# Optimization experiments

Measured on AMD Instinct MI355X. Metric: run time of the kernel, lower is better.

Reference implementation:

```python
import jax, jax.numpy as jnp
import numpy as np

E = 256; D = 512; A = 5; NS = 2048; NQ = 8192; NWAY = 5
_OTHERS = np.array([[j for j in range(A) if j != i] for i in range(A)])  # [A, A-1] indices of other agents
_ROWS = np.arange(A)[:, None]


def _ln(x, g, b, eps=1e-5):
    m = x.mean(-1, keepdims=True)
    v = ((x - m) ** 2).mean(-1, keepdims=True)
    return (x - m) * jax.lax.rsqrt(v + eps) * g + b


def _mha(x, in_w, in_b, out_w, out_b, h, mask=None):
    # torch nn.MultiheadAttention (batch_first) self-attention. in_w: [3E,E], out_w: [E,E]
    B, S, Em = x.shape
    hd = Em // h
    qkv = x @ in_w.T + in_b
    q, k, v = jnp.split(qkv, 3, axis=-1)
    q = q.reshape(B, S, h, hd).transpose(0, 2, 1, 3) * (1.0 / np.sqrt(hd))
    k = k.reshape(B, S, h, hd).transpose(0, 2, 1, 3)
    v = v.reshape(B, S, h, hd).transpose(0, 2, 1, 3)
    s = jnp.einsum('bhqd,bhkd->bhqk', q, k)
    if mask is not None:
        s = jnp.where(mask, s, jnp.asarray(-1e9, s.dtype))
    a = jax.nn.softmax(s, axis=-1)
    o = jnp.einsum('bhqk,bhkd->bhqd', a, v).transpose(0, 2, 1, 3).reshape(B, S, Em)
    return o @ out_w.T + out_b


def _forward(support_x, support_y, query_x, n_way, fe0_w1, fe0_b1, fe0_g1, fe0_be1, fe0_w2, fe0_b2, fe0_g2, fe0_be2, fe1_w1, fe1_b1, fe1_g, fe1_be, fe1_w2, fe1_b2, fe2_w1, fe2_b1, fe2_w2, fe2_b2, fe2_g, fe2_be, fe3_w1, fe3_b1, fe3_w2, fe3_b2, fe3_g, fe3_be, fe4_w1, fe4_b1, fe4_w2, fe4_b2, fe4_w3, fe4_b3, msg_enc_w, msg_enc_b, agg_in_w, agg_in_b, agg_out_w, agg_out_b, proc_w1, proc_b1, proc_w2, proc_b2, internal_state, proto_in_w, proto_in_b, proto_out_w, proto_out_b, cls_w1, cls_b1, cls_w2, cls_b2, cls_w3, cls_b3, comm_w, f_w1, f_b1, f_w2, f_b2, f_w3, f_b3):
    # --- per-agent-type feature extractors (eval mode: dropout off) ---
    def fe0(x):
        h = jax.nn.relu(_ln(x @ fe0_w1 + fe0_b1, fe0_g1, fe0_be1))
        return jax.nn.relu(_ln(h @ fe0_w2 + fe0_b2, fe0_g2, fe0_be2))
    def fe1(x):
        h = jax.nn.relu(_ln(x @ fe1_w1 + fe1_b1, fe1_g, fe1_be))
        return jnp.tanh(h @ fe1_w2 + fe1_b2)
    def fe2(x):
        h = jax.nn.relu(x @ fe2_w1 + fe2_b1)
        return jax.nn.relu(_ln(h @ fe2_w2 + fe2_b2, fe2_g, fe2_be))
    def fe3(x):
        h = jax.nn.relu(x @ fe3_w1 + fe3_b1)
        return jax.nn.sigmoid(_ln(h @ fe3_w2 + fe3_b2, fe3_g, fe3_be))
    def fe4(x):
        h = jax.nn.relu(x @ fe4_w1 + fe4_b1)
        h = jax.nn.relu(h @ fe4_w2 + fe4_b2)
        return h @ fe4_w3 + fe4_b3
    feats_s = jnp.stack([fe0(support_x), fe1(support_x), fe2(support_x), fe3(support_x), fe4(support_x)])  # [A,NS,E]
    feats_q = jnp.stack([fe0(query_x), fe1(query_x), fe2(query_x), fe3(query_x), fe4(query_x)])            # [A,NQ,E]

    # --- one communication round: generate -> weight -> MHA-aggregate -> MLP-process ---
    agent_state = feats_s.mean(1) + internal_state                                         # [A,E]
    messages = jnp.tanh(jnp.einsum('ae,aef->af', agent_state, msg_enc_w) + msg_enc_b)      # [A,E]
    wgt = jax.nn.softmax(comm_w, axis=-1)                                                  # [A,A]
    msgs = messages[_OTHERS] * wgt[_ROWS, _OTHERS][..., None]                              # [A,A-1,E]
    def agg_one(m, iw, ib, ow, ob):
        return _mha(m[None], iw, ib, ow, ob, 4)[0].mean(0)
    agg = jax.vmap(agg_one)(msgs, agg_in_w, agg_in_b, agg_out_w, agg_out_b)                # [A,E]
    comb = internal_state + agg
    hh = jax.nn.relu(jnp.einsum('ae,aef->af', comb, proc_w1) + proc_b1)
    ck = jnp.einsum('ae,aef->af', hh, proc_w2) + proc_b2                                   # [A,E] communicated knowledge

    # --- class-masked prototype attention (equivalent to per-class MHA) + logits ---
    mask = support_y[:, None] == support_y[None, :]                                        # [NS,NS]
    counts = jax.ops.segment_sum(jnp.ones(support_y.shape, jnp.float32), support_y, num_segments=n_way)
    def head(fs, fq, cki, piw, pib, pw, pb, c1, c1b, c2, c2b, c3, c3b):
        att = _mha((fs + cki[None])[None], piw, pib, pw, pb, 2, mask[None, None])[0]       # [NS,E]
        psum = jax.ops.segment_sum(att, support_y, num_segments=n_way)
        protos = jnp.where(counts[:, None] > 0, psum / jnp.maximum(counts, 1.0)[:, None], 0.0)  # [n_way,E]
        eq = jnp.concatenate([fq, jnp.broadcast_to(cki, fq.shape)], axis=-1)               # [NQ,2E]
        d2 = (fq * fq).sum(-1, keepdims=True) + (protos * protos).sum(-1)[None, :] - 2.0 * (fq @ protos.T)
        dist = jnp.sqrt(jnp.maximum(d2, 1e-12))                                            # cdist
        c = jax.nn.relu(eq @ c1 + c1b)
        c = jax.nn.relu(c @ c2 + c2b)
        conf = c @ c3 + c3b                                                                # [NQ,1]
        return -dist + conf * 0.1
    logits = jax.vmap(head)(feats_s, feats_q, ck, proto_in_w, proto_in_b, proto_out_w, proto_out_b, cls_w1, cls_b1, cls_w2, cls_b2, cls_w3, cls_b3)  # [A,NQ,n_way]

    # --- decision fusion over concatenated per-agent query features ---
    qcat = feats_q.transpose(1, 0, 2).reshape(NQ, A * E)
    fh = jax.nn.relu(qcat @ f_w1 + f_b1)
    fh = jax.nn.relu(fh @ f_w2 + f_b2)
    fused = fh @ f_w3 + f_b3                                                               # [NQ,1]
    return logits, fused


def setup_inputs() -> dict:
    key = jax.random.key(0)
    ks = iter(jax.random.split(key, 80))
    def rn(shape, scale=1.0):
        return (jax.random.normal(next(ks), shape) * scale).astype(jnp.float32)
    def lin(shape, fan):
        return rn(shape, 1.0 / np.sqrt(fan))
    z = lambda s: jnp.zeros(s, jnp.float32)
    o = lambda s: jnp.ones(s, jnp.float32)
    inp = {}
    inp['support_x'] = rn((NS, D))
    inp['support_y'] = jax.random.randint(next(ks), (NS,), 0, NWAY, dtype=jnp.int32)
    inp['query_x'] = rn((NQ, D))
    inp['n_way'] = NWAY
    inp['fe0_w1'] = lin((D, 2 * E), D); inp['fe0_b1'] = z((2 * E,)); inp['fe0_g1'] = o((2 * E,)); inp['fe0_be1'] = z((2 * E,))
    inp['fe0_w2'] = lin((2 * E, E), 2 * E); inp['fe0_b2'] = z((E,)); inp['fe0_g2'] = o((E,)); inp['fe0_be2'] = z((E,))
    inp['fe1_w1'] = lin((D, E), D); inp['fe1_b1'] = z((E,)); inp['fe1_g'] = o((E,)); inp['fe1_be'] = z((E,))
    inp['fe1_w2'] = lin((E, E), E); inp['fe1_b2'] = z((E,))
    inp['fe2_w1'] = lin((D, 3 * E), D); inp['fe2_b1'] = z((3 * E,))
    inp['fe2_w2'] = lin((3 * E, E), 3 * E); inp['fe2_b2'] = z((E,)); inp['fe2_g'] = o((E,)); inp['fe2_be'] = z((E,))
    inp['fe3_w1'] = lin((D, E), D); inp['fe3_b1'] = z((E,))
    inp['fe3_w2'] = lin((E, E), E); inp['fe3_b2'] = z((E,)); inp['fe3_g'] = o((E,)); inp['fe3_be'] = z((E,))
    inp['fe4_w1'] = lin((D, 2 * E), D); inp['fe4_b1'] = z((2 * E,))
    inp['fe4_w2'] = lin((2 * E, E), 2 * E); inp['fe4_b2'] = z((E,))
    inp['fe4_w3'] = lin((E, E), E); inp['fe4_b3'] = z((E,))
    inp['msg_enc_w'] = lin((A, E, E), E); inp['msg_enc_b'] = z((A, E))
    inp['agg_in_w'] = lin((A, 3 * E, E), E); inp['agg_in_b'] = z((A, 3 * E))
    inp['agg_out_w'] = lin((A, E, E), E); inp['agg_out_b'] = z((A, E))
    inp['proc_w1'] = lin((A, E, E), E); inp['proc_b1'] = z((A, E))
    inp['proc_w2'] = lin((A, E, E), E); inp['proc_b2'] = z((A, E))
    inp['internal_state'] = rn((A, E), 0.01)
    inp['proto_in_w'] = lin((A, 3 * E, E), E); inp['proto_in_b'] = z((A, 3 * E))
    inp['proto_out_w'] = lin((A, E, E), E); inp['proto_out_b'] = z((A, E))
    inp['cls_w1'] = lin((A, 2 * E, E), 2 * E); inp['cls_b1'] = z((A, E))
    inp['cls_w2'] = lin((A, E, E // 2), E); inp['cls_b2'] = z((A, E // 2))
    inp['cls_w3'] = lin((A, E // 2, 1), E // 2); inp['cls_b3'] = z((A, 1))
    inp['comm_w'] = (jnp.eye(A) * 0.5 + 0.1).astype(jnp.float32)
    inp['f_w1'] = lin((A * E, E), A * E); inp['f_b1'] = z((E,))
    inp['f_w2'] = lin((E, E // 2), E); inp['f_b2'] = z((E // 2,))
    inp['f_w3'] = lin((E // 2, 1), E // 2); inp['f_b3'] = z((1,))
    return inp


def reference(support_x, support_y, query_x, n_way, fe0_w1, fe0_b1, fe0_g1, fe0_be1, fe0_w2, fe0_b2, fe0_g2, fe0_be2, fe1_w1, fe1_b1, fe1_g, fe1_be, fe1_w2, fe1_b2, fe2_w1, fe2_b1, fe2_w2, fe2_b2, fe2_g, fe2_be, fe3_w1, fe3_b1, fe3_w2, fe3_b2, fe3_g, fe3_be, fe4_w1, fe4_b1, fe4_w2, fe4_b2, fe4_w3, fe4_b3, msg_enc_w, msg_enc_b, agg_in_w, agg_in_b, agg_out_w, agg_out_b, proc_w1, proc_b1, proc_w2, proc_b2, internal_state, proto_in_w, proto_in_b, proto_out_w, proto_out_b, cls_w1, cls_b1, cls_w2, cls_b2, cls_w3, cls_b3, comm_w, f_w1, f_b1, f_w2, f_b2, f_w3, f_b3):
    return _forward(support_x, support_y, query_x, n_way, fe0_w1, fe0_b1, fe0_g1, fe0_be1, fe0_w2, fe0_b2, fe0_g2, fe0_be2, fe1_w1, fe1_b1, fe1_g, fe1_be, fe1_w2, fe1_b2, fe2_w1, fe2_b1, fe2_w2, fe2_b2, fe2_g, fe2_be, fe3_w1, fe3_b1, fe3_w2, fe3_b2, fe3_g, fe3_be, fe4_w1, fe4_b1, fe4_w2, fe4_b2, fe4_w3, fe4_b3, msg_enc_w, msg_enc_b, agg_in_w, agg_in_b, agg_out_w, agg_out_b, proc_w1, proc_b1, proc_w2, proc_b2, internal_state, proto_in_w, proto_in_b, proto_out_w, proto_out_b, cls_w1, cls_b1, cls_w2, cls_b2, cls_w3, cls_b3, comm_w, f_w1, f_b1, f_w2, f_b2, f_w3, f_b3)
```

## Files before the change

### kernel.cpp

```cpp
#include <hip/hip_runtime.h>
#include <hip/hip_bf16.h>

typedef __hip_bfloat16 bf16;
typedef short s8v __attribute__((ext_vector_type(8)));
typedef short s4v __attribute__((ext_vector_type(4)));
typedef float f4v __attribute__((ext_vector_type(4)));

#define A_  5
#define D_  512
#define E_  256
#define NS_ 2048
#define NQ_ 8192
#define NM_ 10240
#define NWAY_ 5
#define QSCALE 0.088388347648318447f
#define FSTR ((size_t)NM_ * E_)

__device__ inline float ldw(const void* p, size_t i, int f32) {
  return f32 ? ((const float*)p)[i] : __bfloat162float(((const bf16*)p)[i]);
}
template<bool DYN>
__device__ inline float ldT(const void* p, size_t i, int f32) {
  if (DYN) return ldw(p, i, f32);
  return ((const float*)p)[i];
}

__device__ inline short f2bf(float v) {
  union { float f; unsigned u; } x; x.f = v;
  unsigned r = x.u + 0x7fffu + ((x.u >> 16) & 1u);
  return (short)(r >> 16);
}
__device__ inline float bf2f(short s) {
  union { unsigned u; float f; } x; x.u = ((unsigned)(unsigned short)s) << 16;
  return x.f;
}

struct Ptrs { const void* p[64]; int sz[64]; };

__global__ void probe_k(Ptrs P, int* flags) {
  int b = blockIdx.x, lane = threadIdx.x;
  if (b == 1 || b == 3) { if (lane == 0) flags[b] = 0; return; }
  const bf16* t = (const bf16*)P.p[b];
  int n = P.sz[b];
  int K = (n >> 1) < 64 ? (n >> 1) : 64;
  bool big = false, eNZ = false, oNZ = false;
  if (lane < K) {
    float e = __bfloat162float(t[2 * lane]);
    float o = __bfloat162float(t[2 * lane + 1]);
    big = !(fabsf(e) <= 1e3f);
    eNZ = (e != 0.f); oNZ = (o != 0.f);
  }
  unsigned long long bb = __ballot(big), eb = __ballot(eNZ), ob = __ballot(oNZ);
  if (lane == 0) flags[b] = (bb != 0ull || (eb == 0ull && ob != 0ull)) ? 1 : 0;
}

__global__ void classidx_k(const int* __restrict__ y, int* __restrict__ idx,
                           int* __restrict__ cnt, int* __restrict__ cstart) {
  __shared__ int sc[NWAY_];
  int tid = threadIdx.x;
  if (tid < NWAY_) sc[tid] = 0;
  __syncthreads();
  for (int i = tid; i < NS_; i += 256) {
    int c = y[i];
    int pos = atomicAdd(&sc[c], 1);
    idx[c * NS_ + pos] = i;
  }
  __syncthreads();
  if (tid < NWAY_) cnt[tid] = sc[tid];
  if (tid == 0) { int s = 0; for (int q = 0; q < NWAY_; ++q) { cstart[q] = s; s += sc[q]; } }
}

__global__ void xcopy_k(const void* __restrict__ sx, const void* __restrict__ qx,
                        short* __restrict__ XC, const int* __restrict__ flags) {
  size_t i = ((size_t)blockIdx.x * 256 + threadIdx.x) * 4;
  const size_t SN = (size_t)NS_ * 512;
  if (i < SN) {
    int f = flags[0];
    #pragma unroll
    for (int q = 0; q < 4; ++q) XC[i + q] = f2bf(ldw(sx, i + q, f));
  } else {
    int f = flags[2];
    size_t j = i - SN;
    #pragma unroll
    for (int q = 0; q < 4; ++q) XC[i + q] = f2bf(ldw(qx, j + q, f));
  }
}

__global__ void wcat_k(Ptrs P, short* __restrict__ Wcat, float* __restrict__ bcat,
                       const int* __restrict__ flags) {
  int n = blockIdx.x * 256 + threadIdx.x;
  int k = blockIdx.y;
  int iw, ib, nl, Nloc;
  if (n < 512)       { iw = 4;  ib = 5;  nl = n;        Nloc = 512; }
  else if (n < 768)  { iw = 12; ib = 13; nl = n - 512;  Nloc = 256; }
  else if (n < 1536) { iw = 18; ib = 19; nl = n - 768;  Nloc = 768; }
  else if (n < 1792) { iw = 24; ib = 25; nl = n - 1536; Nloc = 256; }
  else               { iw = 30; ib = 31; nl = n - 1792; Nloc = 512; }
  Wcat[(size_t)n * 512 + k] = f2bf(ldw(P.p[iw], (size_t)k * Nloc + nl, flags[iw]));
  if (k == 0) bcat[n] = ldw(P.p[ib], nl, flags[ib]);
}

__global__ void wcls_k(const void* __restrict__ cw1, const void* __restrict__ fw1,
                       short* __restrict__ B2, const int* __restrict__ flags) {
  int n = blockIdx.x, a = blockIdx.y, k = threadIdx.x;
  float v;
  if (n < 256) v = ldw(cw1, ((size_t)a * 512 + k) * 256 + n, flags[51]);
  else v = ldw(fw1, ((size_t)(a * 256 + k)) * 256 + (n - 256), flags[58]);
  B2[((size_t)a * 512 + n) * 256 + k] = f2bf(v);
}

#define LSTR 40
template<int AMODE, int BMODE, bool DYNBIAS, bool TRB, int ACT, bool ACCUM,
         bool KSPLIT = false, bool OUTBF16 = false, bool DOMAP = false>
__global__ __launch_bounds__(256) void gemm_k(
    const void* __restrict__ A, int lda,
    const void* __restrict__ B, int ldb, size_t offB,
    const void* __restrict__ bias, size_t offBias,
    float* __restrict__ C, int ldc,
    int M, int N, int K, float alpha,
    int ia, int ib, int ibias, const int* __restrict__ flags,
    size_t sA, size_t sB, size_t sBias, size_t sC, size_t kstrideA,
    unsigned long long amap)
{
  const int fA = (AMODE == 1) ? flags[ia] : 1;
  const int fB = (BMODE == 1) ? flags[ib] : 1;
  const int fBi = DYNBIAS ? flags[ibias] : 1;
  const size_t zA = (size_t)blockIdx.z * sA;
  const size_t zB = offB + (size_t)blockIdx.z * sB;
  const size_t zBias = offBias + (size_t)blockIdx.z * sBias;
  float* Cz = C + (size_t)blockIdx.z * sC;
  bf16* Cz16 = (bf16*)C + (size_t)blockIdx.z * sC;
  __shared__ short As[128 * LSTR];
  __shared__ short Bs[128 * LSTR];
  const int tid = threadIdx.x;
  const int bm = blockIdx.y * 128, bn = blockIdx.x * 128;
  const int lane = tid & 63, wid = tid >> 6;
  const int lm = lane & 15, quad = lane >> 4;
  const int wy = (wid >> 1) * 64, wx = (wid & 1) * 64;
  f4v acc[4][4];
  #pragma unroll
  for (int i = 0; i < 4; ++i)
    #pragma unroll
    for (int j = 0; j < 4; ++j) acc[i][j] = (f4v)(0.f);

  const int am = tid >> 1, ah = (tid & 1) * 16;

  s8v a_s0, a_s1;
  float a_f[16];
  s8v b_s0, b_s1;
  float b_f[16];
  short b_h[16];

  auto loadA = [&](int k0) {
    int kk = k0 + ah;
    size_t base;
    if (KSPLIT) base = zA + (size_t)(kk >> 8) * kstrideA + (size_t)(bm + am) * lda + (kk & 255);
    else base = zA + (size_t)(bm + am) * lda + kk;
    if constexpr (AMODE == 2) {
      const bf16* ap = (const bf16*)A + base;
      a_s0 = *(const s8v*)ap;
      a_s1 = *(const s8v*)(ap + 8);
    } else {
      if (fA) {
        const float4* src = (const float4*)((const float*)A + base);
        #pragma unroll
        for (int q = 0; q < 4; ++q) {
          float4 v = src[q];
          a_f[q*4] = v.x; a_f[q*4+1] = v.y; a_f[q*4+2] = v.z; a_f[q*4+3] = v.w;
        }
      } else {
        #pragma unroll
        for (int q = 0; q < 16; ++q) a_f[q] = ldw(A, base + q, 0);
      }
    }
  };
  auto storeA = [&]() {
    if constexpr (AMODE == 2) {
      *(s8v*)&As[am * LSTR + ah] = a_s0;
      *(s8v*)&As[am * LSTR + ah + 8] = a_s1;
    } else {
      short tmp[16];
      #pragma unroll
      for (int q = 0; q < 16; ++q) tmp[q] = f2bf(a_f[q]);
      s4v* dst = (s4v*)&As[am * LSTR + ah];
      #pragma unroll
      for (int q = 0; q < 4; ++q) dst[q] = *(s4v*)&tmp[q*4];
    }
  };
  auto loadB = [&](int k0) {
    if constexpr (TRB) {
      int n = tid >> 1, h = (tid & 1) * 16;
      size_t base = zB + (size_t)(bn + n) * ldb + k0 + h;
      if constexpr (BMODE == 2) {
        const bf16* bp = (const bf16*)B + base;
        b_s0 = *(const s8v*)bp;
        b_s1 = *(const s8v*)(bp + 8);
      } else {
        if (fB) {
          const float4* src = (const float4*)((const float*)B + base);
          #pragma unroll
          for (int q = 0; q < 4; ++q) {
            float4 v = src[q];
            b_f[q*4] = v.x; b_f[q*4+1] = v.y; b_f[q*4+2] = v.z; b_f[q*4+3] = v.w;
          }
        } else {
          #pragma unroll
          for (int q = 0; q < 16; ++q) b_f[q] = ldw(B, base + q, 0);
        }
      }
    } else {
      int n = tid & 127, kk2 = (tid >> 7) * 16;
      #pragma unroll
      for (int j = 0; j < 16; ++j) {
        size_t bi = zB + (size_t)(k0 + kk2 + j) * ldb + bn + n;
        if constexpr (BMODE == 2) b_h[j] = ((const short*)B)[bi];
        else b_f[j] = ldT<BMODE == 1>(B, bi, fB);
      }
    }
  };
  auto storeB = [&]() {
    if constexpr (TRB) {
      int n = tid >> 1, h = (tid & 1) * 16;
      if constexpr (BMODE == 2) {
        *(s8v*)&Bs[n * LSTR + h] = b_s0;
        *(s8v*)&Bs[n * LSTR + h + 8] = b_s1;
      } else {
        short tmp[16];
        #pragma unroll
        for (int q = 0; q < 16; ++q) tmp[q] = f2bf(b_f[q]);
        s4v* dst = (s4v*)&Bs[n * LSTR + h];
        #pragma unroll
        for (int q = 0; q < 4; ++q) dst[q] = *(s4v*)&tmp[q*4];
      }
    } else {
      int n = tid & 127, kk2 = (tid >> 7) * 16;
      short tmp[16];
      #pragma unroll
      for (int j = 0; j < 16; ++j) tmp[j] = (BMODE == 2) ? b_h[j] : f2bf(b_f[j]);
      s4v* dst = (s4v*)&Bs[n * LSTR + kk2];
      #pragma unroll
      for (int q = 0; q < 4; ++q) dst[q] = *(s4v*)&tmp[q*4];
    }
  };

  loadA(0);
  loadB(0);
  for (int k0 = 0; k0 < K; k0 += 32) {
    storeA();
    storeB();
    __syncthreads();
    if (k0 + 32 < K) { loadA(k0 + 32); loadB(k0 + 32); }
    s8v af[4], bfr[4];
    #pragma unroll
    for (int mi = 0; mi < 4; ++mi)
      af[mi] = *(const s8v*)&As[(wy + mi*16 + lm) * LSTR + quad * 8];
    #pragma unroll
    for (int ni = 0; ni < 4; ++ni)
      bfr[ni] = *(const s8v*)&Bs[(wx + ni*16 + lm) * LSTR + quad * 8];
    #pragma unroll
    for (int mi = 0; mi < 4; ++mi)
      #pragma unroll
      for (int ni = 0; ni < 4; ++ni)
        acc[mi][ni] = __builtin_amdgcn_mfma_f32_16x16x32_bf16(af[mi], bfr[ni], acc[mi][ni], 0, 0, 0);
    __syncthreads();
  }
  const int actc = DOMAP ? (int)((amap >> ((bn >> 7) * 2)) & 3ULL) : ACT;
  #pragma unroll
  for (int mi = 0; mi < 4; ++mi) {
    #pragma unroll
    for (int r = 0; r < 4; ++r) {
      int row = bm + wy + mi*16 + quad*4 + r;
      #pragma unroll
      for (int ni = 0; ni < 4; ++ni) {
        int col = bn + wx + ni*16 + lm;
        float v = acc[mi][ni][r] * alpha;
        if (ACCUM) v += Cz[(size_t)row * ldc + col];
        if (bias) v += ldT<DYNBIAS>(bias, zBias + col, fBi);
        if (actc == 1) v = fmaxf(v, 0.f);
        else if (actc == 2) v = tanhf(v);
        else if (actc == 3) v = 1.f / (1.f + expf(-v));
        if (OUTBF16) Cz16[(size_t)row * ldc + col] = __float2bfloat16(v);
        else Cz[(size_t)row * ldc + col] = v;
      }
    }
  }
}

template<int AMODE, int BMODE, bool DYNBIAS, bool TRB, int ACT, bool ACCUM,
         bool KSPLIT = false, bool OUTBF16 = false, bool DOMAP = false>
static void gemm(hipStream_t s, const void* A, int lda, const void* B, int ldb, size_t offB,
                 const void* bias, size_t offBias, float* C, int ldc, int M, int N, int K,
                 float alpha, int ia, int ib, int ibias, const int* flags,
                 int batch = 1, size_t sA = 0, size_t sB = 0, size_t sBias = 0, size_t sC = 0,
                 size_t kstrideA = 0, unsigned long long amap = 0) {
  dim3 g(N / 128, M / 128, batch), b(256);
  gemm_k<AMODE, BMODE, DYNBIAS, TRB, ACT, ACCUM, KSPLIT, OUTBF16, DOMAP><<<g, b, 0, s>>>(
      A, lda, B, ldb, offB, bias, offBias, C, ldc, M, N, K, alpha, ia, ib, ibias, flags,
      sA, sB, sBias, sC, kstrideA, amap);
}

template<int ACT, bool INBF, bool OUTBF>
__global__ __launch_bounds__(256) void ln_k(const void* __restrict__ X, const void* __restrict__ g,
                                            const void* __restrict__ be, void* __restrict__ Y,
                                            int W, int ldx, int ldy,
                                            int ig, int ibe, const int* __restrict__ flags) {
  const int fG = flags[ig], fBe = flags[ibe];
  int row = blockIdx.x;
  const float* xf = (const float*)X + (size_t)row * ldx;
  const bf16* xb = (const bf16*)X + (size_t)row * ldx;
  float* yf = (float*)Y + (size_t)row * ldy;
  bf16* yb = (bf16*)Y + (size_t)row * ldy;
  __shared__ float red[256];
  int tid = threadIdx.x;
  float s1 = 0.f, s2 = 0.f;
  for (int i = tid; i < W; i += 256) {
    float v = INBF ? __bfloat162float(xb[i]) : xf[i];
    s1 += v; s2 += v * v;
  }
  red[tid] = s1; __syncthreads();
  for (int o = 128; o > 0; o >>= 1) { if (tid < o) red[tid] += red[tid + o]; __syncthreads(); }
  float mean = red[0] / W; __syncthreads();
  red[tid] = s2; __syncthreads();
  for (int o = 128; o > 0; o >>= 1) { if (tid < o) red[tid] += red[tid + o]; __syncthreads(); }
  float var = fmaxf(red[0] / W - mean * mean, 0.f);
  float rstd = rsqrtf(var + 1e-5f);
  for (int i = tid; i < W; i += 256) {
    float x = INBF ? __bfloat162float(xb[i]) : xf[i];
    float v = (x - mean) * rstd * ldw(g, i, fG) + ldw(be, i, fBe);
    if (ACT == 1) v = fmaxf(v, 0.f);
    else if (ACT == 3) v = 1.f / (1.f + expf(-v));
    if (OUTBF) yb[i] = __float2bfloat16(v);
    else yf[i] = v;
  }
}

__global__ void statepart_k(const short* __restrict__ featsC, float* __restrict__ part) {
  int a = blockIdx.x, g = blockIdx.y, e = threadIdx.x;
  const short* p = featsC + (size_t)a * FSTR + ((size_t)g * 128) * E_ + e;
  float s = 0.f;
  for (int n = 0; n < 128; ++n) s += bf2f(p[(size_t)n * E_]);
  part[((size_t)a * 16 + g) * E_ + e] = s;
}

__global__ void statecomb_k(const float* __restrict__ part, const void* __restrict__ internal,
                            float* __restrict__ state, const int* __restrict__ flags) {
  int a = blockIdx.x, e = threadIdx.x;
  float s = 0.f;
  for (int g = 0; g < 16; ++g) s += part[((size_t)a * 16 + g) * E_ + e];
  state[a * E_ + e] = s * (1.f / NS_) + ldw(internal, (size_t)a * E_ + e, flags[46]);
}

__global__ void mvpart_k(const float* __restrict__ x, const void* __restrict__ W, int iw,
                         float* __restrict__ part, const int* __restrict__ flags) {
  int a = blockIdx.x, g = blockIdx.y, f = threadIdx.x;
  const int fW = flags[iw];
  float s = 0.f;
  size_t wb = (size_t)a * E_ * E_ + f;
  for (int e = g * 32; e < g * 32 + 32; ++e)
    s += x[a * E_ + e] * ldw(W, wb + (size_t)e * E_, fW);
  part[((size_t)a * 8 + g) * E_ + f] = s;
}

template<int ACT>
__global__ void mvcomb_k(const float* __restrict__ part, const void* __restrict__ b, int ibb,
                         float* __restrict__ y, const int* __restrict__ flags) {
  int a = blockIdx.x, f = threadIdx.x;
  float s = 0.f;
  for (int g = 0; g < 8; ++g) s += part[((size_t)a * 8 + g) * E_ + f];
  s += ldw(b, (size_t)a * E_ + f, flags[ibb]);
  if (ACT == 1) s = fmaxf(s, 0.f);
  else if (ACT == 2) s = tanhf(s);
  y[a * E_ + f] = s;
}

__device__ inline float wave_sum64(float v) {
  for (int o = 32; o > 0; o >>= 1) v += __shfl_down(v, o);
  return v;
}

__global__ __launch_bounds__(256) void qkvcomm_k(const float* __restrict__ msg,
                                                 const void* __restrict__ comm_w,
                                                 const void* __restrict__ in_w,
                                                 const void* __restrict__ in_b,
                                                 float* __restrict__ qkvc,
                                                 const int* __restrict__ flags) {
  const int fCW = flags[57], fIW = flags[38], fIB = flags[39];
  int gw = blockIdx.x * 4 + (threadIdx.x >> 6);
  int a = gw / 768, f = gw % 768;
  int lane = threadIdx.x & 63;
  float w[5]; float mx = -1e30f;
  for (int j = 0; j < 5; ++j) { w[j] = ldw(comm_w, a * 5 + j, fCW); mx = fmaxf(mx, w[j]); }
  float sum = 0.f;
  for (int j = 0; j < 5; ++j) { w[j] = __expf(w[j] - mx); sum += w[j]; }
  for (int j = 0; j < 5; ++j) w[j] /= sum;
  int others[4]; { int c = 0; for (int j = 0; j < 5; ++j) if (j != a) others[c++] = j; }
  int e0 = lane * 4;
  float4 wv;
  size_t b = (size_t)a * 768 * E_ + (size_t)f * E_ + e0;
  if (fIW) wv = *(const float4*)((const float*)in_w + b);
  else wv = make_float4(ldw(in_w, b, 0), ldw(in_w, b + 1, 0), ldw(in_w, b + 2, 0), ldw(in_w, b + 3, 0));
  float acc[4];
  #pragma unroll
  for (int t = 0; t < 4; ++t) {
    const float4 mv = *(const float4*)(msg + others[t] * E_ + e0);
    acc[t] = mv.x * wv.x + mv.y * wv.y + mv.z * wv.z + mv.w * wv.w;
  }
  #pragma unroll
  for (int t = 0; t < 4; ++t) acc[t] = wave_sum64(acc[t]);
  if (lane == 0) {
    float bb = ldw(in_b, (size_t)a * 768 + f, fIB);
    #pragma unroll
    for (int t = 0; t < 4; ++t)
      qkvc[((size_t)a * 4 + t) * 768 + f] = acc[t] * w[others[t]] + bb;
  }
}

__global__ __launch_bounds__(256) void attn4_k(const float* __restrict__ qkvc,
                                               float* __restrict__ obar) {
  int a = blockIdx.x, tid = threadIdx.x;
  __shared__ float qkv[4][768];
  __shared__ float attw[4][16];
// ... 201 lines not shown
    for (int mi = 0; mi < 4; ++mi) {
      #pragma unroll
      for (int r = 0; r < 4; ++r) {
        int lrow = mi * 16 + quad * 4 + r;
        int gi = i0 + lrow;
        if (gi < n) {
          float m = Msm[lrow];
          float invl = 1.f / Lsm[lrow];
          ca += __expf(acc[mi][r] * QSCALE - m) * invl;
        }
      }
    }
  }
  ca += __shfl_xor(ca, 16);
  ca += __shfl_xor(ca, 32);
  int col = j0 + wid * 16 + lm;
  if (quad == 0 && col < n)
    colsum[(size_t)z * NS_ + cstart[c] + col] = ca;
}

#define PCH 8
__global__ __launch_bounds__(1024) void proto_reduce_k(
    const short* __restrict__ qkv_all, const int* __restrict__ idx,
    const int* __restrict__ cnt, const int* __restrict__ cstart,
    const float* __restrict__ colsum, float* __restrict__ proto_pre) {
  int c = blockIdx.x, a = blockIdx.y;
  int n = cnt[c];
  int tid = threadIdx.x, lane = tid & 63, wid = tid >> 6;
  int h = lane >> 5;
  int e0 = lane * 4;
  const short* qkv = qkv_all + (size_t)a * NS_ * 768 + 512;
  const float* csum = colsum + (size_t)(a * 2 + h) * NS_ + cstart[c];
  const int* myidx = idx + c * NS_;
  float a0 = 0.f, a1 = 0.f, a2 = 0.f, a3 = 0.f;
  for (int k = wid; k < n; k += 16) {
    float w = csum[k];
    const s4v v = *(const s4v*)(qkv + (size_t)myidx[k] * 768 + e0);
    a0 += w * bf2f(v[0]); a1 += w * bf2f(v[1]);
    a2 += w * bf2f(v[2]); a3 += w * bf2f(v[3]);
  }
  __shared__ float red[16][E_];
  *(float4*)&red[wid][e0] = make_float4(a0, a1, a2, a3);
  __syncthreads();
  if (tid < E_) {
    float s = 0.f;
    #pragma unroll
    for (int wdx = 0; wdx < 16; ++wdx) s += red[wdx][tid];
    proto_pre[((size_t)a * NWAY_ + c) * E_ + tid] = (n > 0) ? s / (float)n : 0.f;
  }
}

__global__ void proto_outproj_k(const float* __restrict__ proto_pre, const void* __restrict__ ow,
                                const void* __restrict__ ob, const int* __restrict__ cnt,
                                float* __restrict__ protos_all, const int* __restrict__ flags) {
  int c = blockIdx.x, a = blockIdx.y, e = threadIdx.x;
  const int fW = flags[49], fB = flags[50];
  __shared__ float pp[E_];
  pp[e] = proto_pre[((size_t)a * NWAY_ + c) * E_ + e];
  __syncthreads();
  size_t wb = (size_t)a * E_ * E_ + (size_t)e * E_;
  float s = 0.f;
  for (int k = 0; k < E_; ++k) s += pp[k] * ldw(ow, wb + k, fW);
  float v = s + ldw(ob, (size_t)a * E_ + e, fB);
  protos_all[((size_t)a * NWAY_ + c) * E_ + e] = (cnt[c] > 0) ? v : 0.f;
}

__global__ void bias2_k(const float* __restrict__ ck, const void* __restrict__ w1,
                        const void* __restrict__ b1, float* __restrict__ biascat2,
                        const int* __restrict__ flags) {
  const int fW = flags[51], fB = flags[52];
  int a = blockIdx.x, n = threadIdx.x;
  __shared__ float c[E_];
  c[n] = ck[a * E_ + n]; __syncthreads();
  size_t wbase = (size_t)a * 2 * E_ * E_ + (size_t)E_ * E_ + n;
  float s = 0.f;
  for (int k = 0; k < E_; ++k) s += c[k] * ldw(w1, wbase + (size_t)k * E_, fW);
  biascat2[(size_t)a * 512 + n] = s + ldw(b1, (size_t)a * E_ + n, fB);
  biascat2[(size_t)a * 512 + 256 + n] = 0.f;
}

__global__ void fcomb_k(const short* __restrict__ U, const void* __restrict__ b1,
                        short* __restrict__ fh1, const int* __restrict__ flags) {
  int i = blockIdx.x, n = threadIdx.x;
  const int fB = flags[59];
  float s = 0.f;
  #pragma unroll
  for (int a = 0; a < A_; ++a)
    s += bf2f(U[((size_t)a * NQ_ + i) * 512 + 256 + n]);
  s += ldw(b1, n, fB);
  fh1[(size_t)i * 256 + n] = f2bf(fmaxf(s, 0.f));
}

__global__ __launch_bounds__(64) void logits_k(const short* __restrict__ fqbase,
                                               const float* __restrict__ protos_all,
                                               const bf16* __restrict__ c2all,
                                               const void* __restrict__ w3,
                                               const void* __restrict__ b3,
                                               float* __restrict__ out,
                                               const int* __restrict__ flags) {
  const int fW = flags[55], fB = flags[56];
  int i = blockIdx.x, a = blockIdx.y, lane = threadIdx.x;
  const short* fq = fqbase + (size_t)a * FSTR + (size_t)i * E_ + lane * 4;
  const float* protos = protos_all + (size_t)a * NWAY_ * E_;
  const bf16* c2 = c2all + ((size_t)a * NQ_ + i) * 128;
  s4v xv4 = *(const s4v*)fq;
  float x0 = bf2f(xv4[0]), x1 = bf2f(xv4[1]), x2 = bf2f(xv4[2]), x3 = bf2f(xv4[3]);
  float qq = wave_sum64(x0 * x0 + x1 * x1 + x2 * x2 + x3 * x3);
  float cpart = __bfloat162float(c2[lane * 2]) * ldw(w3, (size_t)a * 128 + lane * 2, fW) +
                __bfloat162float(c2[lane * 2 + 1]) * ldw(w3, (size_t)a * 128 + lane * 2 + 1, fW);
  float conf = wave_sum64(cpart);
  if (lane == 0) conf += ldw(b3, a, fB);
  for (int c = 0; c < NWAY_; ++c) {
    float4 pv = ((const float4*)(protos + c * E_))[lane];
    float dt = wave_sum64(x0 * pv.x + x1 * pv.y + x2 * pv.z + x3 * pv.w);
    float pp = wave_sum64(pv.x * pv.x + pv.y * pv.y + pv.z * pv.z + pv.w * pv.w);
    if (lane == 0) {
      float d2 = fmaxf(qq + pp - 2.f * dt, 1e-12f);
      out[((size_t)a * NQ_ + i) * NWAY_ + c] = -sqrtf(d2) + 0.1f * conf;
    }
  }
}

__global__ __launch_bounds__(64) void fused_k(const float* __restrict__ h2, const void* __restrict__ w3,
                                              const void* __restrict__ b3, float* __restrict__ out,
                                              const int* __restrict__ flags) {
  const int fW = flags[62], fB = flags[63];
  int i = blockIdx.x, lane = threadIdx.x;
  float s = h2[(size_t)i * 128 + lane * 2] * ldw(w3, lane * 2, fW) +
            h2[(size_t)i * 128 + lane * 2 + 1] * ldw(w3, lane * 2 + 1, fW);
  s = wave_sum64(s);
  if (lane == 0) out[i] = s + ldw(b3, 0, fB);
}

extern "C" void kernel_launch(void* const* d_in, const int* in_sizes, int n_in,
                              void* d_out, int out_size, void* d_ws, size_t ws_size,
                              hipStream_t stream) {
  (void)out_size; (void)ws_size;
  #define P(i) ((const void*)d_in[i])
  const int* support_y = (const int*)d_in[1];
  float* out = (float*)d_out;

  int* flags = (int*)d_ws;
  char* base = (char*)d_ws + 256;
  short* featsC = (short*)base;
  char* R = base + (size_t)A_ * FSTR * 2;
  short* t1cat   = (short*)R;
  short* qkv_all = (short*)R;
  short* U       = (short*)(R + (size_t)15728640);
  short* fh1     = (short*)R;
  float* fh2     = (float*)(R + (size_t)8388608);
  char* XCR = R + (size_t)57671680;
  short* XC   = (short*)XCR;
  short* tmp2 = (short*)XCR;
  short* b4   = (short*)(XCR + (size_t)NM_ * 256 * 2);
  short* clsC2_all = (short*)XCR;
  char* S = XCR + (size_t)10485760;
  float* state      = (float*)S;
  float* msg        = state + A_ * E_;
  float* ck         = msg + A_ * E_;
  float* protos_all = ck + A_ * E_;
  float* biascat2   = protos_all + A_ * NWAY_ * E_;
  float* ml         = biascat2 + A_ * 512;
  float* colsum     = ml + (size_t)A_ * 2 * NS_ * 2;
  float* proto_pre  = colsum + (size_t)A_ * 2 * NS_;
  int*   idx        = (int*)(proto_pre + A_ * NWAY_ * E_);
  int*   cnt        = idx + NWAY_ * NS_;
  int*   cstart     = cnt + NWAY_;
  float* statepart  = (float*)(cstart + NWAY_ + 3);
  float* mvp        = statepart + A_ * 16 * E_;
  float* qkvc       = mvp + A_ * 8 * E_;
  float* obar       = qkvc + A_ * 4 * 768;
  float* comb       = obar + A_ * E_;
  float* hh         = comb + A_ * E_;
  float* ckb        = hh + A_ * E_;
  float* ppart      = ckb + A_ * 768;
  float* bcat       = ppart + (size_t)A_ * NWAY_ * PCH * E_;
  short* Wcat       = (short*)(bcat + 2304);
  short* Bcat2      = Wcat + (size_t)2304 * 512;

  const short* fq_base = featsC + (size_t)NS_ * E_;

  Ptrs ps;
  for (int i = 0; i < 64; ++i) {
    ps.p[i] = (i < n_in) ? d_in[i] : nullptr;
    ps.sz[i] = (i < n_in) ? in_sizes[i] : 0;
  }
  probe_k<<<64, 64, 0, stream>>>(ps, flags);
  classidx_k<<<1, 256, 0, stream>>>(support_y, idx, cnt, cstart);
  xcopy_k<<<(NM_ * 512 / 4) / 256, 256, 0, stream>>>(P(0), P(2), XC, flags);
  wcat_k<<<dim3(9, 512), 256, 0, stream>>>(ps, Wcat, bcat, flags);
  wcls_k<<<dim3(512, A_), 256, 0, stream>>>(P(51), P(58), Bcat2, flags);

  gemm<2, 2, false, true, 0, false, false, true, true>(
      stream, XC, 512, Wcat, 512, 0, bcat, 0, (float*)t1cat, 2304,
      NM_, 2304, 512, 1.f, -1, -1, -1, flags, 1, 0, 0, 0, 0, 0, 0x555555000ULL);
  ln_k<1, true, true><<<NM_, 256, 0, stream>>>(t1cat, P(6), P(7), t1cat, 512, 2304, 2304, 6, 7, flags);
  gemm<2, 1, true, false, 0, false, false, true>(stream, t1cat, 2304, P(8), 256, 0, P(9), 0,
                                                 (float*)tmp2, 256, NM_, 256, 512, 1.f, -1, 8, 9, flags);
  ln_k<1, true, true><<<NM_, 256, 0, stream>>>(tmp2, P(10), P(11), featsC, 256, 256, 256, 10, 11, flags);
  ln_k<1, true, true><<<NM_, 256, 0, stream>>>(t1cat + 512, P(14), P(15), t1cat + 512, 256, 2304, 2304, 14, 15, flags);
  gemm<2, 1, true, false, 2, false, false, true>(stream, t1cat + 512, 2304, P(16), 256, 0, P(17), 0,
                                                 (float*)(featsC + FSTR), 256, NM_, 256, 256, 1.f, -1, 16, 17, flags);
  gemm<2, 1, true, false, 0, false, false, true>(stream, t1cat + 768, 2304, P(20), 256, 0, P(21), 0,
                                                 (float*)tmp2, 256, NM_, 256, 768, 1.f, -1, 20, 21, flags);
  ln_k<1, true, true><<<NM_, 256, 0, stream>>>(tmp2, P(22), P(23), featsC + 2 * FSTR, 256, 256, 256, 22, 23, flags);
  gemm<2, 1, true, false, 0, false, false, true>(stream, t1cat + 1536, 2304, P(26), 256, 0, P(27), 0,
                                                 (float*)tmp2, 256, NM_, 256, 256, 1.f, -1, 26, 27, flags);
  ln_k<3, true, true><<<NM_, 256, 0, stream>>>(tmp2, P(28), P(29), featsC + 3 * FSTR, 256, 256, 256, 28, 29, flags);
  gemm<2, 1, true, false, 1, false, false, true>(stream, t1cat + 1792, 2304, P(32), 256, 0, P(33), 0,
                                                 (float*)b4, 256, NM_, 256, 512, 1.f, -1, 32, 33, flags);
  gemm<2, 1, true, false, 0, false, false, true>(stream, b4, 256, P(34), 256, 0, P(35), 0,
                                                 (float*)(featsC + 4 * FSTR), 256, NM_, 256, 256, 1.f, -1, 34, 35, flags);

  statepart_k<<<dim3(A_, 16), 256, 0, stream>>>(featsC, statepart);
  statecomb_k<<<A_, 256, 0, stream>>>(statepart, P(46), state, flags);
  mvpart_k<<<dim3(A_, 8), 256, 0, stream>>>(state, P(36), 36, mvp, flags);
  mvcomb_k<2><<<A_, 256, 0, stream>>>(mvp, P(37), 37, msg, flags);
  qkvcomm_k<<<A_ * 768 / 4, 256, 0, stream>>>(msg, P(57), P(38), P(39), qkvc, flags);
  attn4_k<<<A_, 256, 0, stream>>>(qkvc, obar);
  combproj_k<<<A_ * E_ / 4, 256, 0, stream>>>(obar, P(40), P(41), P(46), comb, flags);
  mvpart_k<<<dim3(A_, 8), 256, 0, stream>>>(comb, P(42), 42, mvp, flags);
  mvcomb_k<1><<<A_, 256, 0, stream>>>(mvp, P(43), 43, hh, flags);
  mvpart_k<<<dim3(A_, 8), 256, 0, stream>>>(hh, P(44), 44, mvp, flags);
  mvcomb_k<0><<<A_, 256, 0, stream>>>(mvp, P(45), 45, ck, flags);

  ckb_k<<<A_ * 768 / 4, 256, 0, stream>>>(ck, P(47), P(48), ckb, flags);
  gemm<2, 1, false, true, 0, false, false, true>(stream, featsC, 256, P(47), 256, 0, ckb, 0,
                                    (float*)qkv_all, 768, NS_, 768, 256, 1.f, -1, 47, -1, flags,
                                    A_, FSTR, (size_t)3 * E_ * E_, (size_t)768, (size_t)NS_ * 768);
  {
    dim3 g(NWAY_, NS_ / 64, A_ * 2);
    attn_stats_k<<<g, 256, 0, stream>>>(qkv_all, idx, cnt, cstart, ml);
    attn_colsum_k<<<g, 256, 0, stream>>>(qkv_all, idx, cnt, cstart, ml, colsum);
  }
  proto_reduce_k<<<dim3(NWAY_, A_), 1024, 0, stream>>>(qkv_all, idx, cnt, cstart, colsum, proto_pre);
  proto_outproj_k<<<dim3(NWAY_, A_), 256, 0, stream>>>(proto_pre, P(49), P(50), cnt, protos_all, flags);
  bias2_k<<<A_, 256, 0, stream>>>(ck, P(51), P(52), biascat2, flags);

  gemm<2, 2, false, true, 0, false, false, true, true>(
      stream, fq_base, 256, Bcat2, 256, 0, biascat2, 0, (float*)U, 512,
      NQ_, 512, 256, 1.f, -1, -1, -1, flags,
      A_, FSTR, (size_t)512 * 256, (size_t)512, (size_t)NQ_ * 512, 0, 0x5ULL);
  fcomb_k<<<NQ_, 256, 0, stream>>>(U, P(59), fh1, flags);

  gemm<2, 1, true, false, 1, false, false, true>(stream, U, 512, P(53), 128, 0,
                                     P(54), 0, (float*)clsC2_all, 128, NQ_, 128, 256, 1.f, -1, 53, 54, flags,
                                     A_, (size_t)NQ_ * 512, (size_t)E_ * 128, (size_t)128, (size_t)NQ_ * 128);
  logits_k<<<dim3(NQ_, A_), 64, 0, stream>>>(fq_base, protos_all, (const bf16*)clsC2_all, P(55), P(56), out, flags);

  gemm<2, 1, true, false, 1, false>(stream, fh1, 256, P(60), 128, 0, P(61), 0, fh2, 128, NQ_, 128, 256, 1.f, -1, 60, 61, flags);
  fused_k<<<NQ_, 64, 0, stream>>>(fh2, P(62), P(63), out + (size_t)A_ * NQ_ * NWAY_, flags);
}
```

Before: 915.1 us.

## Use direct global-to-LDS loads in bf16 GEMM, merge matvec kernels, precompute prototype norms

When both GEMM operands are bf16 and B is transposed, tiles are now staged with global_load_lds straight into double-buffered shared memory. This drops the register round-trip and one barrier per k-step. The split matvec (partial plus combine) kernels are merged into one kernel that stages x in shared memory, removing three launches. Prototype squared norms are computed once in proto_outproj and read in logits_k instead of being recomputed by a wave reduction per query. The risks are unpadded LDS rows (stride 32), which can cause bank conflicts, and lower parallelism in the merged matvec, which now uses only 5 blocks.

```diff
diff --git a/kernel.cpp b/kernel.cpp
--- a/kernel.cpp
+++ b/kernel.cpp
@@ -33,6 +33,12 @@
 __device__ inline float bf2f(short s) {
   union { unsigned u; float f; } x; x.u = ((unsigned)(unsigned short)s) << 16;
   return x.f;
+}
+
+__device__ __forceinline__ void gload16(const void* g, void* l) {
+  __builtin_amdgcn_global_load_lds(
+      (const __attribute__((address_space(1))) unsigned int*)g,
+      (__attribute__((address_space(3))) unsigned int*)l, 16, 0, 0);
 }
 
 struct Ptrs { const void* p[64]; int sz[64]; };
@@ -122,6 +128,7 @@
     size_t sA, size_t sB, size_t sBias, size_t sC, size_t kstrideA,
     unsigned long long amap)
 {
+  constexpr bool GDB = (AMODE == 2) && (BMODE == 2) && TRB && !KSPLIT;
   const int fA = (AMODE == 1) ? flags[ia] : 1;
   const int fB = (BMODE == 1) ? flags[ib] : 1;
   const int fBi = DYNBIAS ? flags[ibias] : 1;
@@ -130,8 +137,6 @@
   const size_t zBias = offBias + (size_t)blockIdx.z * sBias;
   float* Cz = C + (size_t)blockIdx.z * sC;
   bf16* Cz16 = (bf16*)C + (size_t)blockIdx.z * sC;
-  __shared__ short As[128 * LSTR];
-  __shared__ short Bs[128 * LSTR];
   const int tid = threadIdx.x;
   const int bm = blockIdx.y * 128, bn = blockIdx.x * 128;
   const int lane = tid & 63, wid = tid >> 6;
@@ -143,127 +148,169 @@
     #pragma unroll
     for (int j = 0; j < 4; ++j) acc[i][j] = (f4v)(0.f);
 
-  const int am = tid >> 1, ah = (tid & 1) * 16;
-
-  s8v a_s0, a_s1;
-  float a_f[16];
-  s8v b_s0, b_s1;
-  float b_f[16];
-  short b_h[16];
-
-  auto loadA = [&](int k0) {
-    int kk = k0 + ah;
-    size_t base;
-    if (KSPLIT) base = zA + (size_t)(kk >> 8) * kstrideA + (size_t)(bm + am) * lda + (kk & 255);
-    else base = zA + (size_t)(bm + am) * lda + kk;
-    if constexpr (AMODE == 2) {
-      const bf16* ap = (const bf16*)A + base;
-      a_s0 = *(const s8v*)ap;
-      a_s1 = *(const s8v*)(ap + 8);
-    } else {
-      if (fA) {
-        const float4* src = (const float4*)((const float*)A + base);
+  if constexpr (GDB) {
+    __shared__ short smem[4 * 128 * 32];
+    const int srow = lane >> 2, scol = (lane & 3) * 8;
+    const short* Azs = (const short*)A + zA;
+    const short* Bzs = (const short*)B + zB;
+    auto stage = [&](int bsel, int k0) {
+      short* Asb = smem + bsel * 4096;
+      short* Bsb = smem + 8192 + bsel * 4096;
+      #pragma unroll
+      for (int q = 0; q < 2; ++q) {
+        int rb = (wid * 2 + q) * 16;
+        gload16(Azs + (size_t)(bm + rb + srow) * lda + k0 + scol, Asb + rb * 32);
+        gload16(Bzs + (size_t)(bn + rb + srow) * ldb + k0 + scol, Bsb + rb * 32);
+      }
+    };
+    stage(0, 0);
+    __syncthreads();
+    int cur = 0;
+    for (int k0 = 0; k0 < K; k0 += 32) {
+      if (k0 + 32 < K) stage(cur ^ 1, k0 + 32);
+      const short* Asb = smem + cur * 4096;
+      const short* Bsb = smem + 8192 + cur * 4096;
+      s8v af[4], bfr[4];
+      #pragma unroll
+      for (int mi = 0; mi < 4; ++mi)
+        af[mi] = *(const s8v*)&Asb[(wy + mi*16 + lm) * 32 + quad * 8];
+      #pragma unroll
+      for (int ni = 0; ni < 4; ++ni)
+        bfr[ni] = *(const s8v*)&Bsb[(wx + ni*16 + lm) * 32 + quad * 8];
+      #pragma unroll
+      for (int mi = 0; mi < 4; ++mi)
         #pragma unroll
-        for (int q = 0; q < 4; ++q) {
-          float4 v = src[q];
-          a_f[q*4] = v.x; a_f[q*4+1] = v.y; a_f[q*4+2] = v.z; a_f[q*4+3] = v.w;
-        }
+        for (int ni = 0; ni < 4; ++ni)
+          acc[mi][ni] = __builtin_amdgcn_mfma_f32_16x16x32_bf16(af[mi], bfr[ni], acc[mi][ni], 0, 0, 0);
+      __syncthreads();
+      cur ^= 1;
+    }
+  } else {
+    __shared__ short As[128 * LSTR];
+    __shared__ short Bs[128 * LSTR];
+    const int am = tid >> 1, ah = (tid & 1) * 16;
+
+    s8v a_s0, a_s1;
+    float a_f[16];
+    s8v b_s0, b_s1;
+    float b_f[16];
+    short b_h[16];
+
+    auto loadA = [&](int k0) {
+      int kk = k0 + ah;
+      size_t base;
+      if (KSPLIT) base = zA + (size_t)(kk >> 8) * kstrideA + (size_t)(bm + am) * lda + (kk & 255);
+      else base = zA + (size_t)(bm + am) * lda + kk;
+      if constexpr (AMODE == 2) {
+        const bf16* ap = (const bf16*)A + base;
+        a_s0 = *(const s8v*)ap;
+        a_s1 = *(const s8v*)(ap + 8);
       } else {
-        #pragma unroll
-        for (int q = 0; q < 16; ++q) a_f[q] = ldw(A, base + q, 0);
-      }
-    }
-  };
-  auto storeA = [&]() {
-    if constexpr (AMODE == 2) {
-      *(s8v*)&As[am * LSTR + ah] = a_s0;
-      *(s8v*)&As[am * LSTR + ah + 8] = a_s1;
-    } else {
-      short tmp[16];
-      #pragma unroll
-      for (int q = 0; q < 16; ++q) tmp[q] = f2bf(a_f[q]);
-      s4v* dst = (s4v*)&As[am * LSTR + ah];
-      #pragma unroll
-      for (int q = 0; q < 4; ++q) dst[q] = *(s4v*)&tmp[q*4];
-    }
-  };
-  auto loadB = [&](int k0) {
-    if constexpr (TRB) {
-      int n = tid >> 1, h = (tid & 1) * 16;
-      size_t base = zB + (size_t)(bn + n) * ldb + k0 + h;
-      if constexpr (BMODE == 2) {
-        const bf16* bp = (const bf16*)B + base;
-        b_s0 = *(const s8v*)bp;
-        b_s1 = *(const s8v*)(bp + 8);
-      } else {
-        if (fB) {
-          const float4* src = (const float4*)((const float*)B + base);
+        if (fA) {
+          const float4* src = (const float4*)((const float*)A + base);
           #pragma unroll
           for (int q = 0; q < 4; ++q) {
             float4 v = src[q];
-            b_f[q*4] = v.x; b_f[q*4+1] = v.y; b_f[q*4+2] = v.z; b_f[q*4+3] = v.w;
+            a_f[q*4] = v.x; a_f[q*4+1] = v.y; a_f[q*4+2] = v.z; a_f[q*4+3] = v.w;
           }
         } else {
           #pragma unroll
-          for (int q = 0; q < 16; ++q) b_f[q] = ldw(B, base + q, 0);
+          for (int q = 0; q < 16; ++q) a_f[q] = ldw(A, base + q, 0);
         }
       }
-    } else {
-      int n = tid & 127, kk2 = (tid >> 7) * 16;
-      #pragma unroll
-      for (int j = 0; j < 16; ++j) {
-        size_t bi = zB + (size_t)(k0 + kk2 + j) * ldb + bn + n;
-        if constexpr (BMODE == 2) b_h[j] = ((const short*)B)[bi];
-        else b_f[j] = ldT<BMODE == 1>(B, bi, fB);
-      }
-    }
-  };
-  auto storeB = [&]() {
-    if constexpr (TRB) {
-      int n = tid >> 1, h = (tid & 1) * 16;
-      if constexpr (BMODE == 2) {
-        *(s8v*)&Bs[n * LSTR + h] = b_s0;
-        *(s8v*)&Bs[n * LSTR + h + 8] = b_s1;
+    };
+    auto storeA = [&]() {
+      if constexpr (AMODE == 2) {
+        *(s8v*)&As[am * LSTR + ah] = a_s0;
+        *(s8v*)&As[am * LSTR + ah + 8] = a_s1;
       } else {
         short tmp[16];
         #pragma unroll
-        for (int q = 0; q < 16; ++q) tmp[q] = f2bf(b_f[q]);
-        s4v* dst = (s4v*)&Bs[n * LSTR + h];
+        for (int q = 0; q < 16; ++q) tmp[q] = f2bf(a_f[q]);
+        s4v* dst = (s4v*)&As[am * LSTR + ah];
         #pragma unroll
         for (int q = 0; q < 4; ++q) dst[q] = *(s4v*)&tmp[q*4];
       }
-    } else {
-      int n = tid & 127, kk2 = (tid >> 7) * 16;
-      short tmp[16];
-      #pragma unroll
-      for (int j = 0; j < 16; ++j) tmp[j] = (BMODE == 2) ? b_h[j] : f2bf(b_f[j]);
-      s4v* dst = (s4v*)&Bs[n * LSTR + kk2];
-      #pragma unroll
-      for (int q = 0; q < 4; ++q) dst[q] = *(s4v*)&tmp[q*4];
+    };
+    auto loadB = [&](int k0) {
+      if constexpr (TRB) {
+        int n = tid >> 1, h = (tid & 1) * 16;
+        size_t base = zB + (size_t)(bn + n) * ldb + k0 + h;
+        if constexpr (BMODE == 2) {
+          const bf16* bp = (const bf16*)B + base;
+          b_s0 = *(const s8v*)bp;
+          b_s1 = *(const s8v*)(bp + 8);
+        } else {
+          if (fB) {
+            const float4* src = (const float4*)((const float*)B + base);
+            #pragma unroll
+            for (int q = 0; q < 4; ++q) {
+              float4 v = src[q];
+              b_f[q*4] = v.x; b_f[q*4+1] = v.y; b_f[q*4+2] = v.z; b_f[q*4+3] = v.w;
+            }
+          } else {
+            #pragma unroll
+            for (int q = 0; q < 16; ++q) b_f[q] = ldw(B, base + q, 0);
+          }
+        }
+      } else {
+        int n = tid & 127, kk2 = (tid >> 7) * 16;
+        #pragma unroll
+        for (int j = 0; j < 16; ++j) {
+          size_t bi = zB + (size_t)(k0 + kk2 + j) * ldb + bn + n;
+          if constexpr (BMODE == 2) b_h[j] = ((const short*)B)[bi];
+          else b_f[j] = ldT<BMODE == 1>(B, bi, fB);
+        }
+      }
+    };
+    auto storeB = [&]() {
+      if constexpr (TRB) {
+        int n = tid >> 1, h = (tid & 1) * 16;
+        if constexpr (BMODE == 2) {
+          *(s8v*)&Bs[n * LSTR + h] = b_s0;
+          *(s8v*)&Bs[n * LSTR + h + 8] = b_s1;
+        } else {
+          short tmp[16];
+          #pragma unroll
+          for (int q = 0; q < 16; ++q) tmp[q] = f2bf(b_f[q]);
+          s4v* dst = (s4v*)&Bs[n * LSTR + h];
+          #pragma unroll
+          for (int q = 0; q < 4; ++q) dst[q] = *(s4v*)&tmp[q*4];
+        }
+      } else {
+        int n = tid & 127, kk2 = (tid >> 7) * 16;
+        short tmp[16];
+        #pragma unroll
+        for (int j = 0; j < 16; ++j) tmp[j] = (BMODE == 2) ? b_h[j] : f2bf(b_f[j]);
+        s4v* dst = (s4v*)&Bs[n * LSTR + kk2];
+        #pragma unroll
+        for (int q = 0; q < 4; ++q) dst[q] = *(s4v*)&tmp[q*4];
+      }
+    };
+
+    loadA(0);
+    loadB(0);
+    for (int k0 = 0; k0 < K; k0 += 32) {
+      storeA();
+      storeB();
+      __syncthreads();
+      if (k0 + 32 < K) { loadA(k0 + 32); loadB(k0 + 32); }
+      s8v af[4], bfr[4];
+      #pragma unroll
+      for (int mi = 0; mi < 4; ++mi)
+        af[mi] = *(const s8v*)&As[(wy + mi*16 + lm) * LSTR + quad * 8];
+      #pragma unroll
+      for (int ni = 0; ni < 4; ++ni)
+        bfr[ni] = *(const s8v*)&Bs[(wx + ni*16 + lm) * LSTR + quad * 8];
+      #pragma unroll
+      for (int mi = 0; mi < 4; ++mi)
+        #pragma unroll
+        for (int ni = 0; ni < 4; ++ni)
+          acc[mi][ni] = __builtin_amdgcn_mfma_f32_16x16x32_bf16(af[mi], bfr[ni], acc[mi][ni], 0, 0, 0);
+      __syncthreads();
     }
-  };
-
-  loadA(0);
-  loadB(0);
-  for (int k0 = 0; k0 < K; k0 += 32) {
-    storeA();
-    storeB();
-    __syncthreads();
-    if (k0 + 32 < K) { loadA(k0 + 32); loadB(k0 + 32); }
-    s8v af[4], bfr[4];
-    #pragma unroll
-    for (int mi = 0; mi < 4; ++mi)
-      af[mi] = *(const s8v*)&As[(wy + mi*16 + lm) * LSTR + quad * 8];
-    #pragma unroll
-    for (int ni = 0; ni < 4; ++ni)
-      bfr[ni] = *(const s8v*)&Bs[(wx + ni*16 + lm) * LSTR + quad * 8];
-    #pragma unroll
-    for (int mi = 0; mi < 4; ++mi)
-      #pragma unroll
-      for (int ni = 0; ni < 4; ++ni)
-        acc[mi][ni] = __builtin_amdgcn_mfma_f32_16x16x32_bf16(af[mi], bfr[ni], acc[mi][ni], 0, 0, 0);
-    __syncthreads();
-  }
+  }
+
   const int actc = DOMAP ? (int)((amap >> ((bn >> 7) * 2)) & 3ULL) : ACT;
   #pragma unroll
   for (int mi = 0; mi < 4; ++mi) {
@@ -350,23 +397,20 @@
   state[a * E_ + e] = s * (1.f / NS_) + ldw(internal, (size_t)a * E_ + e, flags[46]);
 }
 
-__global__ void mvpart_k(const float* __restrict__ x, const void* __restrict__ W, int iw,
-                         float* __restrict__ part, const int* __restrict__ flags) {
-  int a = blockIdx.x, g = blockIdx.y, f = threadIdx.x;
+template<int ACT>
+__global__ __launch_bounds__(256) void mv_k(const float* __restrict__ x, const void* __restrict__ W,
+                                            int iw, const void* __restrict__ b, int ibb,
+                                            float* __restrict__ y, const int* __restrict__ flags) {
+  int a = blockIdx.x, f = threadIdx.x;
   const int fW = flags[iw];
+  __shared__ float xs[E_];
+  xs[f] = x[a * E_ + f];
+  __syncthreads();
   float s = 0.f;
   size_t wb = (size_t)a * E_ * E_ + f;
-  for (int e = g * 32; e < g * 32 + 32; ++e)
-    s += x[a * E_ + e] * ldw(W, wb + (size_t)e * E_, fW);
-  part[((size_t)a * 8 + g) * E_ + f] = s;
-}
-
-template<int ACT>
-__global__ void mvcomb_k(const float* __restrict__ part, const void* __restrict__ b, int ibb,
-                         float* __restrict__ y, const int* __restrict__ flags) {
-  int a = blockIdx.x, f = threadIdx.x;
-  float s = 0.f;
-  for (int g = 0; g < 8; ++g) s += part[((size_t)a * 8 + g) * E_ + f];
+  #pragma unroll 4
+  for (int e = 0; e < E_; ++e)
+    s += xs[e] * ldw(W, wb + (size_t)e * E_, fW);
   s += ldw(b, (size_t)a * E_ + f, flags[ibb]);
   if (ACT == 1) s = fmaxf(s, 0.f);
   else if (ACT == 2) s = tanhf(s);
@@ -674,17 +718,24 @@
 
 __global__ void proto_outproj_k(const float* __restrict__ proto_pre, const void* __restrict__ ow,
                                 const void* __restrict__ ob, const int* __restrict__ cnt,
-                                float* __restrict__ protos_all, const int* __restrict__ flags) {
+                                float* __restrict__ protos_all, float* __restrict__ pnorm,
+                                const int* __restrict__ flags) {
   int c = blockIdx.x, a = blockIdx.y, e = threadIdx.x;
   const int fW = flags[49], fB = flags[50];
   __shared__ float pp[E_];
+  __shared__ float r2[E_];
   pp[e] = proto_pre[((size_t)a * NWAY_ + c) * E_ + e];
   __syncthreads();
   size_t wb = (size_t)a * E_ * E_ + (size_t)e * E_;
   float s = 0.f;
   for (int k = 0; k < E_; ++k) s += pp[k] * ldw(ow, wb + k, fW);
   float v = s + ldw(ob, (size_t)a * E_ + e, fB);
-  protos_all[((size_t)a * NWAY_ + c) * E_ + e] = (cnt[c] > 0) ? v : 0.f;
+  float vm = (cnt[c] > 0) ? v : 0.f;
+  protos_all[((size_t)a * NWAY_ + c) * E_ + e] = vm;
+  r2[e] = vm * vm;
+  __syncthreads();
+  for (int o = 128; o > 0; o >>= 1) { if (e < o) r2[e] += r2[e + o]; __syncthreads(); }
+  if (e == 0) pnorm[a * NWAY_ + c] = r2[0];
 }
 
 __global__ void bias2_k(const float* __restrict__ ck, const void* __restrict__ w1,
@@ -715,6 +766,7 @@
 
 __global__ __launch_bounds__(64) void logits_k(const short* __restrict__ fqbase,
                                                const float* __restrict__ protos_all,
+                                               const float* __restrict__ pnorm,
                                                const bf16* __restrict__ c2all,
                                                const void* __restrict__ w3,
                                                const void* __restrict__ b3,
@@ -735,8 +787,8 @@
   for (int c = 0; c < NWAY_; ++c) {
     float4 pv = ((const float4*)(protos + c * E_))[lane];
     float dt = wave_sum64(x0 * pv.x + x1 * pv.y + x2 * pv.z + x3 * pv.w);
-    float pp = wave_sum64(pv.x * pv.x + pv.y * pv.y + pv.z * pv.z + pv.w * pv.w);
     if (lane == 0) {
+      float pp = pnorm[a * NWAY_ + c];
       float d2 = fmaxf(qq + pp - 2.f * dt, 1e-12f);
       out[((size_t)a * NQ_ + i) * NWAY_ + c] = -sqrtf(d2) + 0.1f * conf;
     }
@@ -836,15 +888,12 @@
 
   statepart_k<<<dim3(A_, 16), 256, 0, stream>>>(featsC, statepart);
   statecomb_k<<<A_, 256, 0, stream>>>(statepart, P(46), state, flags);
-  mvpart_k<<<dim3(A_, 8), 256, 0, stream>>>(state, P(36), 36, mvp, flags);
-  mvcomb_k<2><<<A_, 256, 0, stream>>>(mvp, P(37), 37, msg, flags);
+  mv_k<2><<<A_, 256, 0, stream>>>(state, P(36), 36, P(37), 37, msg, flags);
   qkvcomm_k<<<A_ * 768 / 4, 256, 0, stream>>>(msg, P(57), P(38), P(39), qkvc, flags);
   attn4_k<<<A_, 256, 0, stream>>>(qkvc, obar);
   combproj_k<<<A_ * E_ / 4, 256, 0, stream>>>(obar, P(40), P(41), P(46), comb, flags);
-  mvpart_k<<<dim3(A_, 8), 256, 0, stream>>>(comb, P(42), 42, mvp, flags);
-  mvcomb_k<1><<<A_, 256, 0, stream>>>(mvp, P(43), 43, hh, flags);
-  mvpart_k<<<dim3(A_, 8), 256, 0, stream>>>(hh, P(44), 44, mvp, flags);
-  mvcomb_k<0><<<A_, 256, 0, stream>>>(mvp, P(45), 45, ck, flags);
+  mv_k<1><<<A_, 256, 0, stream>>>(comb, P(42), 42, P(43), 43, hh, flags);
+  mv_k<0><<<A_, 256, 0, stream>>>(hh, P(44), 44, P(45), 45, ck, flags);
 
   ckb_k<<<A_ * 768 / 4, 256, 0, stream>>>(ck, P(47), P(48), ckb, flags);
   gemm<2, 1, false, true, 0, false, false, true>(stream, featsC, 256, P(47), 256, 0, ckb, 0,
@@ -856,7 +905,7 @@
     attn_colsum_k<<<g, 256, 0, stream>>>(qkv_all, idx, cnt, cstart, ml, colsum);
   }
   proto_reduce_k<<<dim3(NWAY_, A_), 1024, 0, stream>>>(qkv_all, idx, cnt, cstart, colsum, proto_pre);
-  proto_outproj_k<<<dim3(NWAY_, A_), 256, 0, stream>>>(proto_pre, P(49), P(50), cnt, protos_all, flags);
+  proto_outproj_k<<<dim3(NWAY_, A_), 256, 0, stream>>>(proto_pre, P(49), P(50), cnt, protos_all, ppart, flags);
   bias2_k<<<A_, 256, 0, stream>>>(ck, P(51), P(52), biascat2, flags);
 
   gemm<2, 2, false, true, 0, false, false, true, true>(
@@ -868,7 +917,7 @@
   gemm<2, 1, true, false, 1, false, false, true>(stream, U, 512, P(53), 128, 0,
                                      P(54), 0, (float*)clsC2_all, 128, NQ_, 128, 256, 1.f, -1, 53, 54, flags,
                                      A_, (size_t)NQ_ * 512, (size_t)E_ * 128, (size_t)128, (size_t)NQ_ * 128);
-  logits_k<<<dim3(NQ_, A_), 64, 0, stream>>>(fq_base, protos_all, (const bf16*)clsC2_all, P(55), P(56), out, flags);
+  logits_k<<<dim3(NQ_, A_), 64, 0, stream>>>(fq_base, protos_all, ppart, (const bf16*)clsC2_all, P(55), P(56), out, flags);
 
   gemm<2, 1, true, false, 1, false>(stream, fh1, 256, P(60), 128, 0, P(61), 0, fh2, 128, NQ_, 128, 256, 1.f, -1, 60, 61, flags);
   fused_k<<<NQ_, 64, 0, stream>>>(fh2, P(62), P(63), out + (size_t)A_ * NQ_ * NWAY_, flags);
```

New measurement: 957.2 us. 4.6% more time.
